# Optimization experiments

Measured on AMD Instinct MI355X. Metric: run time of the kernel, lower is better.

The kernel has to match this reference:

```python
import jax, jax.numpy as jnp
import numpy as np

NUM_STAGES = 2
DE_NEIGHBORS = 3

def _square_distance(a, b):
    # a: [B,N,3], b: [B,S,3] -> [B,N,S] squared euclidean distances
    return (jnp.sum(a * a, axis=-1)[:, :, None]
            + jnp.sum(b * b, axis=-1)[:, None, :]
            - 2.0 * jnp.einsum('bnc,bsc->bns', a, b))

def _propagate(xyz1, xyz2, points1, points2, k):
    # xyz1:[B,N,3] fine, xyz2:[B,S,3] coarse, points1:[B,D1,N], points2:[B,D2,S]
    p2 = jnp.transpose(points2, (0, 2, 1))  # [B,S,D2]
    B, N, _ = xyz1.shape
    S = xyz2.shape[1]
    if S == 1:
        interp = jnp.broadcast_to(p2, (B, N, p2.shape[-1]))
    else:
        d = _square_distance(xyz1, xyz2)              # [B,N,S]
        neg_top, idx = jax.lax.top_k(-d, k)           # k smallest distances
        dists = -neg_top                              # [B,N,k]
        recip = 1.0 / (dists + 1e-8)
        weight = recip / jnp.sum(recip, axis=2, keepdims=True)  # [B,N,k]
        # gather neighbor features: [B,N,k,D2]
        gathered = jnp.take_along_axis(p2[:, None, :, :], idx[..., None], axis=2)
        interp = jnp.sum(gathered * weight[..., None], axis=2)  # [B,N,D2]
    if points1 is not None:
        p1 = jnp.transpose(points1, (0, 2, 1))        # [B,N,D1]
        new = jnp.concatenate([p1, interp], axis=-1)
    else:
        new = interp
    return jnp.transpose(new, (0, 2, 1))              # [B,D1+D2,N]

def setup_inputs() -> dict:
    key = jax.random.key(0)
    ks = jax.random.split(key, 6)
    return {
        'xyz0': jax.random.normal(ks[0], (4, 8192, 3), dtype=jnp.float32),
        'xyz1': jax.random.normal(ks[1], (4, 2048, 3), dtype=jnp.float32),
        'xyz2': jax.random.normal(ks[2], (4, 512, 3), dtype=jnp.float32),
        'x0': jax.random.normal(ks[3], (4, 128, 8192), dtype=jnp.float32),
        'x1': jax.random.normal(ks[4], (4, 256, 2048), dtype=jnp.float32),
        'x2': jax.random.normal(ks[5], (4, 512, 512), dtype=jnp.float32),
    }

def reference(xyz0, xyz1, xyz2, x0, x1, x2):
    # original forward reverses the lists; emulate with pre-reversed lists
    xyz_list = [xyz2, xyz1, xyz0]   # coarse -> fine
    x_list = [x2, x1, x0]
    x = x_list[0]
    for i in range(NUM_STAGES):
        x = _propagate(xyz_list[i + 1], xyz_list[i], x_list[i + 1], x, DE_NEIGHBORS)
    return x  # [4, 896, 8192]
```

## Files before the change

### kernel.cpp

```cpp
#include <hip/hip_runtime.h>

#define BIG 3.0e38f

typedef float vf4 __attribute__((ext_vector_type(4)));

__device__ __forceinline__ void insert3(float d, int s,
                                        float& d0, float& d1, float& d2,
                                        int& i0, int& i1, int& i2) {
    const bool b0 = d < d0;
    const bool b1 = d < d1;
    const bool b2 = d < d2;
    d2 = b1 ? d1 : (b2 ? d : d2);
    i2 = b1 ? i1 : (b2 ? s : i2);
    d1 = b0 ? d0 : (b1 ? d : d1);
    i1 = b0 ? i0 : (b1 ? s : i1);
    d0 = b0 ? d : d0;
    i0 = b0 ? s : i0;
}

template <int S>
__device__ void knn_tile(const float* __restrict__ xyzF, const float* __restrict__ xyzC,
                         int N, int b, int nb,
                         int* __restrict__ idx, float* __restrict__ w,
                         void* smem) {
    constexpr int SPC = S / 8;
    float4* sc  = (float4*)smem;
    float*  smd = (float*)((char*)smem + S * 16);
    int*    smi = (int*)((char*)smem + S * 16 + 3072);
    const int tid = threadIdx.x;

    for (int i = tid; i < S; i += 256) {
        const float x = xyzC[(b * S + i) * 3 + 0];
        const float y = xyzC[(b * S + i) * 3 + 1];
        const float z = xyzC[(b * S + i) * 3 + 2];
        sc[i] = make_float4(x, y, z, x * x + y * y + z * z);
    }
    __syncthreads();

    const int q  = tid & 31;
    const int sp = tid >> 5;
    const int n  = nb + q;
    const float ax = xyzF[(b * N + n) * 3 + 0];
    const float ay = xyzF[(b * N + n) * 3 + 1];
    const float az = xyzF[(b * N + n) * 3 + 2];
    const float an = ax * ax + ay * ay + az * az;

    float d0 = BIG, d1 = BIG, d2 = BIG;
    int i0 = 0, i1 = 0, i2 = 0;
    const int s0 = sp * SPC;
#pragma unroll 8
    for (int s = s0; s < s0 + SPC; ++s) {
        const float4 p = sc[s];
        const float t = ax * p.x + ay * p.y + az * p.z;
        const float d = an + p.w - 2.0f * t;
        insert3(d, s, d0, d1, d2, i0, i1, i2);
    }

    smd[tid * 3 + 0] = d0; smi[tid * 3 + 0] = i0;
    smd[tid * 3 + 1] = d1; smi[tid * 3 + 1] = i1;
    smd[tid * 3 + 2] = d2; smi[tid * 3 + 2] = i2;
    __syncthreads();

    if (tid < 32) {
        float e0 = BIG, e1 = BIG, e2 = BIG;
        int j0 = 0, j1 = 0, j2 = 0;
#pragma unroll
        for (int ch = 0; ch < 8; ++ch) {
#pragma unroll
            for (int k = 0; k < 3; ++k) {
                insert3(smd[(ch * 32 + tid) * 3 + k], smi[(ch * 32 + tid) * 3 + k],
                        e0, e1, e2, j0, j1, j2);
            }
        }
        const float r0 = 1.0f / (e0 + 1e-8f);
        const float r1 = 1.0f / (e1 + 1e-8f);
        const float r2 = 1.0f / (e2 + 1e-8f);
        const float rs = r0 + r1 + r2;
        const int nn = nb + tid;
        idx[(b * 3 + 0) * N + nn] = j0;
        idx[(b * 3 + 1) * N + nn] = j1;
        idx[(b * 3 + 2) * N + nn] = j2;
        w[(b * 3 + 0) * N + nn] = r0 / rs;
        w[(b * 3 + 1) * N + nn] = r1 / rs;
        w[(b * 3 + 2) * N + nn] = r2 / rs;
    }
}

__device__ void transpose_tile(const float* __restrict__ in, float* __restrict__ out,
                               int C, int N, int OS,
                               int b, int nb, int cb, void* smem) {
    float (*s)[65] = (float (*)[65])smem;
    const int lo = threadIdx.x & 63;
    const int r  = threadIdx.x >> 6;
#pragma unroll
    for (int i = 0; i < 16; ++i) {
        const int cl = r + 4 * i;
        s[cl][lo] = in[((size_t)b * C + cb + cl) * N + nb + lo];
    }
    __syncthreads();
#pragma unroll
    for (int i = 0; i < 16; ++i) {
        const int pl = r + 4 * i;
        out[((size_t)b * N + nb + pl) * OS + cb + lo] = s[lo][pl];
    }
}

__global__ __launch_bounds__(256) void k1_stage(const float* __restrict__ xyz0,
                                                const float* __restrict__ xyz1,
                                                const float* __restrict__ xyz2,
                                                const float* __restrict__ x0,
                                                const float* __restrict__ x1,
                                                const float* __restrict__ x2,
                                                float* __restrict__ x1P,
                                                float* __restrict__ x2P,
                                                int* __restrict__ idx1,
                                                float* __restrict__ w1,
                                                int* __restrict__ idx2,
                                                float* __restrict__ w2,
                                                float* __restrict__ out) {
    __shared__ float4 smem4[2432];
    const int id = blockIdx.x;
    const int g  = id / 9;
    const int r9 = id - g * 9;
    if (r9 < 4) {
        const int kid = g * 4 + r9;
        const int b  = kid >> 8;
        const int nb = (kid & 255) * 32;
        knn_tile<2048>(xyz0, xyz1, 8192, b, nb, idx2, w2, smem4);
    } else {
        const int mid = g * 5 + (r9 - 4);
        if (mid < 256) {
            const int b  = mid >> 6;
            const int nb = (mid & 63) * 32;
            knn_tile<512>(xyz1, xyz2, 2048, b, nb, idx1, w1, smem4);
        } else if (mid < 512) {
            const int r  = mid - 256;
            const int b  = r >> 6;
            const int nb = (r & 7) * 64;
            const int cb = ((r >> 3) & 7) * 64;
            transpose_tile(x2, x2P, 512, 512, 512, b, nb, cb, smem4);
        } else if (mid < 1024) {
            const int r  = mid - 512;
            const int b  = r >> 7;
            const int nb = (r & 31) * 64;
            const int cb = ((r >> 5) & 3) * 64;
            transpose_tile(x1, x1P, 256, 2048, 256, b, nb, cb, smem4);
        } else {
            const int r  = mid - 1024;
            const int b  = r >> 6;
            const int lb = r & 63;
            const vf4* src = (const vf4*)x0;
            vf4* dst = (vf4*)out;
#pragma unroll
            for (int t = 0; t < 16; ++t) {
                const int i = lb * 4096 + t * 256 + threadIdx.x;
                const vf4 v = __builtin_nontemporal_load(&src[(size_t)b * (128 * 2048) + i]);
                __builtin_nontemporal_store(v, &dst[(size_t)b * (896 * 2048) + i]);
            }
        }
    }
}

__global__ __launch_bounds__(256) void final_fused(const float* __restrict__ x1P,
                                                   const float* __restrict__ x2P,
                                                   const int* __restrict__ idx1,
                                                   const float* __restrict__ w1,
                                                   const int* __restrict__ idx2,
                                                   const float* __restrict__ w2,
                                                   float* __restrict__ out) {
    __shared__ float tile[64][65];
    __shared__ int   sj[9][64];
    __shared__ float sw[9][64];
    const int id  = blockIdx.x;
    const int xcd = id & 7;
    const int b   = xcd >> 1;
    const int local = ((id >> 3) << 1) | (xcd & 1);
    const int ntile = local / 12;
    const int ctile = local - ntile * 12;
    const int nb  = ntile * 64;
    const int tid = threadIdx.x;

    if (ctile < 4) {
        if (tid < 192) {
            const int p = tid & 63, k = tid >> 6;
            sj[k][p] = idx2[(b * 3 + k) * 8192 + nb + p];
            sw[k][p] = w2[(b * 3 + k) * 8192 + nb + p];
        }
        __syncthreads();
        const int cb = ctile * 64;
        {
            const int c = tid & 63, r = tid >> 6;
            const float* xb = x1P + (size_t)b * 2048 * 256 + cb + c;
#pragma unroll
            for (int i = 0; i < 16; ++i) {
                const int p = r + 4 * i;
                const float v = sw[0][p] * xb[(size_t)sj[0][p] * 256]
                              + sw[1][p] * xb[(size_t)sj[1][p] * 256]
                              + sw[2][p] * xb[(size_t)sj[2][p] * 256];
                tile[p][c] = v;
            }
        }
        __syncthreads();
        {
            const int p = tid & 63, r = tid >> 6;
#pragma unroll
            for (int i = 0; i < 16; ++i) {
                const int cl = r + 4 * i;
                __builtin_nontemporal_store(tile[p][cl],
                    &out[((size_t)b * 896 + 128 + cb + cl) * 8192 + nb + p]);
            }
        }
    } else {
        if (tid < 192) {
            const int p = tid & 63, k = tid >> 6;
            const int   j  = idx2[(b * 3 + k) * 8192 + nb + p];
            const float wk = w2[(b * 3 + k) * 8192 + nb + p];
#pragma unroll
            for (int m = 0; m < 3; ++m) {
                sj[k * 3 + m][p] = idx1[(b * 3 + m) * 2048 + j];
                sw[k * 3 + m][p] = wk * w1[(b * 3 + m) * 2048 + j];
            }
        }
        __syncthreads();
        const int cb = (ctile - 4) * 64;
        {
            const int c = tid & 63, r = tid >> 6;
            const float* xb = x2P + (size_t)b * 512 * 512 + cb + c;
#pragma unroll
            for (int i = 0; i < 16; ++i) {
                const int p = r + 4 * i;
                float v = 0.0f;
#pragma unroll
                for (int j = 0; j < 9; ++j) {
                    v += sw[j][p] * xb[(size_t)sj[j][p] * 512];
                }
                tile[p][c] = v;
            }
        }
        __syncthreads();
        {
            const int p = tid & 63, r = tid >> 6;
#pragma unroll
            for (int i = 0; i < 16; ++i) {
                const int cl = r + 4 * i;
                __builtin_nontemporal_store(tile[p][cl],
                    &out[((size_t)b * 896 + 384 + cb + cl) * 8192 + nb + p]);
            }
        }
    }
}

extern "C" void kernel_launch(void* const* d_in, const int* in_sizes, int n_in,
                              void* d_out, int out_size, void* d_ws, size_t ws_size,
                              hipStream_t stream) {
    const float* xyz0 = (const float*)d_in[0];
    const float* xyz1 = (const float*)d_in[1];
    const float* xyz2 = (const float*)d_in[2];
    const float* x0   = (const float*)d_in[3];
    const float* x1   = (const float*)d_in[4];
    const float* x2   = (const float*)d_in[5];
    float* out = (float*)d_out;

    char* ws = (char*)d_ws;
    float* x1P  = (float*)(ws + 0);
    float* x2P  = (float*)(ws + 8388608);
    int*   idx1 = (int*)(ws + 12582912);
    float* w1   = (float*)(ws + 12681216);
    int*   idx2 = (int*)(ws + 12779520);
    float* w2   = (float*)(ws + 13172736);

    k1_stage<<<dim3(2304), 256, 0, stream>>>(xyz0, xyz1, xyz2, x0, x1, x2,
                                             x1P, x2P, idx1, w1, idx2, w2, out);
    final_fused<<<dim3(6144), 256, 0, stream>>>(x1P, x2P, idx1, w1, idx2, w2, out);
}
```

Before: 218.3 us.

## Merge final gather tiles per point block and use med3 in top-3 insert

The final kernel now gives each block one 64-point tile and loops over all 12 channel tiles, so the index/weight composition is loaded once per point tile rather than once per channel tile. Grid size drops from 6144 to 512 blocks. The top-3 insertion uses fmed3/fmin for the distance updates, and the k1_stage block interleaving (groups of 9) is replaced by contiguous ranges. The fused kernel has fewer blocks and serialises channel tiles with extra barriers, which may hurt latency hiding and occupancy on a GPU with many CUs.

```diff
diff --git a/kernel.cpp b/kernel.cpp
--- a/kernel.cpp
+++ b/kernel.cpp
@@ -10,12 +10,13 @@
     const bool b0 = d < d0;
     const bool b1 = d < d1;
     const bool b2 = d < d2;
-    d2 = b1 ? d1 : (b2 ? d : d2);
     i2 = b1 ? i1 : (b2 ? s : i2);
-    d1 = b0 ? d0 : (b1 ? d : d1);
     i1 = b0 ? i0 : (b1 ? s : i1);
-    d0 = b0 ? d : d0;
-    i0 = b0 ? s : i0;
+    i0 = b0 ? s  : i0;
+    const float nd1 = __builtin_amdgcn_fmed3f(d, d0, d1);
+    d2 = __builtin_amdgcn_fmed3f(d, d1, d2);
+    d0 = fminf(d, d0);
+    d1 = nd1;
 }
 
 template <int S>
@@ -120,89 +121,91 @@
                                                 float* __restrict__ out) {
     __shared__ float4 smem4[2432];
     const int id = blockIdx.x;
-    const int g  = id / 9;
-    const int r9 = id - g * 9;
-    if (r9 < 4) {
-        const int kid = g * 4 + r9;
-        const int b  = kid >> 8;
-        const int nb = (kid & 255) * 32;
+    if (id < 1024) {
+        const int b  = id >> 8;
+        const int nb = (id & 255) * 32;
         knn_tile<2048>(xyz0, xyz1, 8192, b, nb, idx2, w2, smem4);
+    } else if (id < 1280) {
+        const int r  = id - 1024;
+        const int b  = r >> 6;
+        const int nb = (r & 63) * 32;
+        knn_tile<512>(xyz1, xyz2, 2048, b, nb, idx1, w1, smem4);
+    } else if (id < 1536) {
+        const int r  = id - 1280;
+        const int b  = r >> 6;
+        const int nb = (r & 7) * 64;
+        const int cb = ((r >> 3) & 7) * 64;
+        transpose_tile(x2, x2P, 512, 512, 512, b, nb, cb, smem4);
+    } else if (id < 2048) {
+        const int r  = id - 1536;
+        const int b  = r >> 7;
+        const int nb = (r & 31) * 64;
+        const int cb = ((r >> 5) & 3) * 64;
+        transpose_tile(x1, x1P, 256, 2048, 256, b, nb, cb, smem4);
     } else {
-        const int mid = g * 5 + (r9 - 4);
-        if (mid < 256) {
-            const int b  = mid >> 6;
-            const int nb = (mid & 63) * 32;
-            knn_tile<512>(xyz1, xyz2, 2048, b, nb, idx1, w1, smem4);
-        } else if (mid < 512) {
-            const int r  = mid - 256;
-            const int b  = r >> 6;
-            const int nb = (r & 7) * 64;
-            const int cb = ((r >> 3) & 7) * 64;
-            transpose_tile(x2, x2P, 512, 512, 512, b, nb, cb, smem4);
-        } else if (mid < 1024) {
-            const int r  = mid - 512;
-            const int b  = r >> 7;
-            const int nb = (r & 31) * 64;
-            const int cb = ((r >> 5) & 3) * 64;
-            transpose_tile(x1, x1P, 256, 2048, 256, b, nb, cb, smem4);
-        } else {
-            const int r  = mid - 1024;
-            const int b  = r >> 6;
-            const int lb = r & 63;
-            const vf4* src = (const vf4*)x0;
-            vf4* dst = (vf4*)out;
-#pragma unroll
-            for (int t = 0; t < 16; ++t) {
-                const int i = lb * 4096 + t * 256 + threadIdx.x;
-                const vf4 v = __builtin_nontemporal_load(&src[(size_t)b * (128 * 2048) + i]);
-                __builtin_nontemporal_store(v, &dst[(size_t)b * (896 * 2048) + i]);
-            }
-        }
-    }
-}
-
-__global__ __launch_bounds__(256) void final_fused(const float* __restrict__ x1P,
-                                                   const float* __restrict__ x2P,
-                                                   const int* __restrict__ idx1,
-                                                   const float* __restrict__ w1,
-                                                   const int* __restrict__ idx2,
-                                                   const float* __restrict__ w2,
-                                                   float* __restrict__ out) {
+        const int r  = id - 2048;
+        const int b  = r >> 6;
+        const int lb = r & 63;
+        const vf4* src = (const vf4*)x0;
+        vf4* dst = (vf4*)out;
+#pragma unroll
+        for (int t = 0; t < 16; ++t) {
+            const int i = lb * 4096 + t * 256 + threadIdx.x;
+            const vf4 v = __builtin_nontemporal_load(&src[(size_t)b * (128 * 2048) + i]);
+            __builtin_nontemporal_store(v, &dst[(size_t)b * (896 * 2048) + i]);
+        }
+    }
+}
+
+__global__ __launch_bounds__(256) void final_unified(const float* __restrict__ x1P,
+                                                     const float* __restrict__ x2P,
+                                                     const int* __restrict__ idx1,
+                                                     const float* __restrict__ w1,
+                                                     const int* __restrict__ idx2,
+                                                     const float* __restrict__ w2,
+                                                     float* __restrict__ out) {
     __shared__ float tile[64][65];
-    __shared__ int   sj[9][64];
-    __shared__ float sw[9][64];
+    __shared__ int   sj1[3][64];
+    __shared__ float sw1[3][64];
+    __shared__ int   sj9[9][64];
+    __shared__ float sw9[9][64];
     const int id  = blockIdx.x;
     const int xcd = id & 7;
     const int b   = xcd >> 1;
-    const int local = ((id >> 3) << 1) | (xcd & 1);
-    const int ntile = local / 12;
-    const int ctile = local - ntile * 12;
+    const int ntile = ((id >> 3) << 1) | (xcd & 1);
     const int nb  = ntile * 64;
     const int tid = threadIdx.x;
 
-    if (ctile < 4) {
-        if (tid < 192) {
-            const int p = tid & 63, k = tid >> 6;
-            sj[k][p] = idx2[(b * 3 + k) * 8192 + nb + p];
-            sw[k][p] = w2[(b * 3 + k) * 8192 + nb + p];
-        }
-        __syncthreads();
-        const int cb = ctile * 64;
+    if (tid < 192) {
+        const int p = tid & 63, k = tid >> 6;
+        const int   j  = idx2[(b * 3 + k) * 8192 + nb + p];
+        const float wk = w2[(b * 3 + k) * 8192 + nb + p];
+        sj1[k][p] = j * 256;
+        sw1[k][p] = wk;
+#pragma unroll
+        for (int m = 0; m < 3; ++m) {
+            sj9[k * 3 + m][p] = idx1[(b * 3 + m) * 2048 + j] * 512;
+            sw9[k * 3 + m][p] = wk * w1[(b * 3 + m) * 2048 + j];
+        }
+    }
+    __syncthreads();
+
+    const int c = tid & 63;
+    const int r = tid >> 6;
+
+    for (int ct = 0; ct < 4; ++ct) {
+        const int cb = ct * 64;
+        const float* xb = x1P + (size_t)b * 2048 * 256 + cb + c;
+#pragma unroll 8
+        for (int i = 0; i < 16; ++i) {
+            const int p = r + 4 * i;
+            tile[p][c] = sw1[0][p] * xb[sj1[0][p]]
+                       + sw1[1][p] * xb[sj1[1][p]]
+                       + sw1[2][p] * xb[sj1[2][p]];
+        }
+        __syncthreads();
         {
-            const int c = tid & 63, r = tid >> 6;
-            const float* xb = x1P + (size_t)b * 2048 * 256 + cb + c;
-#pragma unroll
-            for (int i = 0; i < 16; ++i) {
-                const int p = r + 4 * i;
-                const float v = sw[0][p] * xb[(size_t)sj[0][p] * 256]
-                              + sw[1][p] * xb[(size_t)sj[1][p] * 256]
-                              + sw[2][p] * xb[(size_t)sj[2][p] * 256];
-                tile[p][c] = v;
-            }
-        }
-        __syncthreads();
-        {
-            const int p = tid & 63, r = tid >> 6;
+            const int p = tid & 63;
 #pragma unroll
             for (int i = 0; i < 16; ++i) {
                 const int cl = r + 4 * i;
@@ -210,36 +213,25 @@
                     &out[((size_t)b * 896 + 128 + cb + cl) * 8192 + nb + p]);
             }
         }
-    } else {
-        if (tid < 192) {
-            const int p = tid & 63, k = tid >> 6;
-            const int   j  = idx2[(b * 3 + k) * 8192 + nb + p];
-            const float wk = w2[(b * 3 + k) * 8192 + nb + p];
-#pragma unroll
-            for (int m = 0; m < 3; ++m) {
-                sj[k * 3 + m][p] = idx1[(b * 3 + m) * 2048 + j];
-                sw[k * 3 + m][p] = wk * w1[(b * 3 + m) * 2048 + j];
-            }
-        }
-        __syncthreads();
-        const int cb = (ctile - 4) * 64;
+        __syncthreads();
+    }
+
+    for (int ct = 0; ct < 8; ++ct) {
+        const int cb = ct * 64;
+        const float* xb = x2P + (size_t)b * 512 * 512 + cb + c;
+#pragma unroll 4
+        for (int i = 0; i < 16; ++i) {
+            const int p = r + 4 * i;
+            float v = 0.0f;
+#pragma unroll
+            for (int j = 0; j < 9; ++j) {
+                v += sw9[j][p] * xb[sj9[j][p]];
+            }
+            tile[p][c] = v;
+        }
+        __syncthreads();
         {
-            const int c = tid & 63, r = tid >> 6;
-            const float* xb = x2P + (size_t)b * 512 * 512 + cb + c;
-#pragma unroll
-            for (int i = 0; i < 16; ++i) {
-                const int p = r + 4 * i;
-                float v = 0.0f;
-#pragma unroll
-                for (int j = 0; j < 9; ++j) {
-                    v += sw[j][p] * xb[(size_t)sj[j][p] * 512];
-                }
-                tile[p][c] = v;
-            }
-        }
-        __syncthreads();
-        {
-            const int p = tid & 63, r = tid >> 6;
+            const int p = tid & 63;
 #pragma unroll
             for (int i = 0; i < 16; ++i) {
                 const int cl = r + 4 * i;
@@ -247,6 +239,7 @@
                     &out[((size_t)b * 896 + 384 + cb + cl) * 8192 + nb + p]);
             }
         }
+        __syncthreads();
     }
 }
 
@@ -271,5 +264,5 @@
 
     k1_stage<<<dim3(2304), 256, 0, stream>>>(xyz0, xyz1, xyz2, x0, x1, x2,
                                              x1P, x2P, idx1, w1, idx2, w2, out);
-    final_fused<<<dim3(6144), 256, 0, stream>>>(x1P, x2P, idx1, w1, idx2, w2, out);
-}
+    final_unified<<<dim3(512), 256, 0, stream>>>(x1P, x2P, idx1, w1, idx2, w2, out);
+}
```

After: 248.9 us. +14.0%, slower.
